# Optimization experiments

Hardware: AMD Instinct MI355X
Metric: run time of the kernel (lower is better)

Reference implementation:

```python
import jax, jax.numpy as jnp
import numpy as np

N_SAMPLES = 131072
N_FEATURES = 512
N_KERNELS = 29


def setup_inputs() -> dict:
    key = jax.random.key(0)
    k1, k2, k3 = jax.random.split(key, 3)
    Xs = jax.random.normal(k1, (N_SAMPLES, N_FEATURES), dtype=jnp.float32)
    Xt = jax.random.normal(k2, (N_SAMPLES, N_FEATURES), dtype=jnp.float32)
    # unit-sum random betas, as in the torch default constructor
    r = jax.random.uniform(k3, (N_KERNELS, 1), dtype=jnp.float32)
    betas = r / jnp.sum(r)
    return {"Xs": Xs, "Xt": Xt, "betas": betas}


def reference(Xs, Xt, betas):
    # default length-scales: gammas = 2 ** arange(-3.5, 3.75, 0.25) -> 29 kernels
    gammas = jnp.power(jnp.float32(2.0), jnp.arange(-3.5, 3.75, 0.25, dtype=jnp.float32))  # [29]

    n, f = Xs.shape
    m = (n // 2) * 2  # drop last sample if odd
    X = Xs[:m].reshape(m // 2, 2, f)  # pairs (x_{2i-1}, x_{2i})
    Y = Xt[:m].reshape(m // 2, 2, f)  # pairs (y_{2i-1}, y_{2i})

    def sq_dist(a, b):  # [P, F] -> [P]
        d = a - b
        return jnp.sum(d * d, axis=1)

    # quadruple v_i = [x, x', y, y']; distances (x,x'), (y,y'), (x,y'), (x',y)
    D = jnp.stack(
        [
            sq_dist(X[:, 0], X[:, 1]),
            sq_dist(Y[:, 0], Y[:, 1]),
            sq_dist(X[:, 0], Y[:, 1]),
            sq_dist(X[:, 1], Y[:, 0]),
        ],
        axis=1,
    )  # [P, 4]

    # K[g, p, c] = exp(-D[p, c] / (2 * gamma_g^2)) -- all 29 kernels in one broadcast
    inv_two_gamma_sq = 1.0 / (2.0 * gammas * gammas)  # [29]
    K = jnp.exp(-D[None, :, :] * inv_two_gamma_sq[:, None, None])  # [29, P, 4]

    h_u = K[..., 0] + K[..., 1] - K[..., 2] - K[..., 3]  # [29, P]
    hat_d = jnp.mean(h_u, axis=1, keepdims=True)  # [29, 1]
    return (betas.T @ hat_d).squeeze(0)  # shape (1,)
```

## Files before the change

kernel.cpp:

```cpp
#include <hip/hip_runtime.h>

#define N_SAMPLES 131072
#define N_FEAT    512
#define N_PAIRS   (N_SAMPLES / 2)
#define N_KER     29
#define PAIR_F    (2 * N_FEAT)

#define NB_MAIN   1024
#define NW_MAIN   (NB_MAIN * 4)
#define CPW_MAIN  (N_PAIRS / NW_MAIN)

struct Batch {
  float4 x0, x1, xp0, xp1, y0, y1, yp0, yp1;
};

__device__ __forceinline__ void load_batch(const float* __restrict__ Xs,
                                           const float* __restrict__ Xt,
                                           int p, int o0, Batch& b) {
  const float* x = Xs + (size_t)p * PAIR_F;
  const float* y = Xt + (size_t)p * PAIR_F;
  b.x0  = *reinterpret_cast<const float4*>(x + o0);
  b.x1  = *reinterpret_cast<const float4*>(x + o0 + 256);
  b.xp0 = *reinterpret_cast<const float4*>(x + o0 + N_FEAT);
  b.xp1 = *reinterpret_cast<const float4*>(x + o0 + N_FEAT + 256);
  b.y0  = *reinterpret_cast<const float4*>(y + o0);
  b.y1  = *reinterpret_cast<const float4*>(y + o0 + 256);
  b.yp0 = *reinterpret_cast<const float4*>(y + o0 + N_FEAT);
  b.yp1 = *reinterpret_cast<const float4*>(y + o0 + N_FEAT + 256);
}

__device__ __forceinline__ void compute_pair(const Batch& b, double c, int lane,
                                             double& acc) {
  double d0 = 0.0, d1 = 0.0, d2 = 0.0, d3 = 0.0;

#define MMD_ACC(A, AP, B, BP)                                   \
  {                                                             \
    const double ax  = (double)(A);                             \
    const double axp = (double)(AP);                            \
    const double ay  = (double)(B);                             \
    const double ayp = (double)(BP);                            \
    double t;                                                   \
    t = ax - axp; d0 = fma(t, t, d0);                           \
    t = ay - ayp; d1 = fma(t, t, d1);                           \
    t = ax - ayp; d2 = fma(t, t, d2);                           \
    t = axp - ay; d3 = fma(t, t, d3);                           \
  }
  MMD_ACC(b.x0.x, b.xp0.x, b.y0.x, b.yp0.x)
  MMD_ACC(b.x0.y, b.xp0.y, b.y0.y, b.yp0.y)
  MMD_ACC(b.x0.z, b.xp0.z, b.y0.z, b.yp0.z)
  MMD_ACC(b.x0.w, b.xp0.w, b.y0.w, b.yp0.w)
  MMD_ACC(b.x1.x, b.xp1.x, b.y1.x, b.yp1.x)
  MMD_ACC(b.x1.y, b.xp1.y, b.y1.y, b.yp1.y)
  MMD_ACC(b.x1.z, b.xp1.z, b.y1.z, b.yp1.z)
  MMD_ACC(b.x1.w, b.xp1.w, b.y1.w, b.yp1.w)
#undef MMD_ACC

#pragma unroll
  for (int s = 32; s > 0; s >>= 1) {
    d0 += __shfl_xor(d0, s);
    d1 += __shfl_xor(d1, s);
    d2 += __shfl_xor(d2, s);
    d3 += __shfl_xor(d3, s);
  }

  if (lane < N_KER) {
    acc += exp(-d0 * c) + exp(-d1 * c) - exp(-d2 * c) - exp(-d3 * c);
  }
}

__device__ __forceinline__ void block_reduce_store(double acc, int lane, int wib,
                                                   int tid, double* __restrict__ ws) {
  __shared__ double sacc[4][32];
  if (lane < 32) sacc[wib][lane] = (lane < N_KER) ? acc : 0.0;
  __syncthreads();
  if (tid < 32) {
    const double s = sacc[0][tid] + sacc[1][tid] + sacc[2][tid] + sacc[3][tid];
    ws[(size_t)blockIdx.x * 32 + tid] = s;
  }
}

__global__ __launch_bounds__(256) void mmd_partial_main(
    const float* __restrict__ Xs, const float* __restrict__ Xt,
    double* __restrict__ ws) {
  const int tid  = threadIdx.x;
  const int lane = tid & 63;
  const int wib  = tid >> 6;
  const int gw   = blockIdx.x * 4 + wib;
  const int o0   = lane * 4;

  const double c = exp2(6.0 - 0.5 * (double)lane);
  double acc = 0.0;

  int pl = gw;
  Batch A, B, C;
  load_batch(Xs, Xt, pl, o0, A); pl += NW_MAIN;
  load_batch(Xs, Xt, pl, o0, B); pl += NW_MAIN;

#pragma unroll 1
  for (int it = 0; it < (CPW_MAIN - 4) / 3; ++it) {
    load_batch(Xs, Xt, pl, o0, C); pl += NW_MAIN;
    compute_pair(A, c, lane, acc);
    load_batch(Xs, Xt, pl, o0, A); pl += NW_MAIN;
    compute_pair(B, c, lane, acc);
    load_batch(Xs, Xt, pl, o0, B); pl += NW_MAIN;
    compute_pair(C, c, lane, acc);
  }
  load_batch(Xs, Xt, pl, o0, C); pl += NW_MAIN;
  compute_pair(A, c, lane, acc);
  load_batch(Xs, Xt, pl, o0, A);
  compute_pair(B, c, lane, acc);
  compute_pair(C, c, lane, acc);
  compute_pair(A, c, lane, acc);

  block_reduce_store(acc, lane, wib, tid, ws);
}

__global__ __launch_bounds__(256) void mmd_partial_fb(
    const float* __restrict__ Xs, const float* __restrict__ Xt,
    double* __restrict__ ws, int nwaves) {
  const int tid  = threadIdx.x;
  const int lane = tid & 63;
  const int wib  = tid >> 6;
  const int gw   = blockIdx.x * 4 + wib;
  const int o0   = lane * 4;

  const double c = exp2(6.0 - 0.5 * (double)lane);
  double acc = 0.0;

  int p = gw;
  if (p < N_PAIRS) {
    Batch A, B;
    load_batch(Xs, Xt, p, o0, A);
    int pn = p + nwaves;
    bool pendingA = true;
    while (pn < N_PAIRS) {
      load_batch(Xs, Xt, pn, o0, B);
      compute_pair(A, c, lane, acc);
      pn += nwaves;
      if (pn < N_PAIRS) {
        load_batch(Xs, Xt, pn, o0, A);
        compute_pair(B, c, lane, acc);
        pn += nwaves;
      } else {
        compute_pair(B, c, lane, acc);
        pendingA = false;
        break;
      }
    }
    if (pendingA) compute_pair(A, c, lane, acc);
  }

  block_reduce_store(acc, lane, wib, tid, ws);
}

__global__ __launch_bounds__(1024) void mmd_final(
    const double* __restrict__ ws, const float* __restrict__ betas,
    float* __restrict__ out, int nb) {
  const int tid = threadIdx.x;
  double acc = 0.0;
  const int total = nb * 32;
  for (int i = tid; i < total; i += 1024) {
    const int g = i & 31;
    if (g < N_KER) acc += (double)betas[g] * ws[i];
  }
  __shared__ double s[1024];
  s[tid] = acc;
  __syncthreads();
  for (int ofs = 512; ofs > 0; ofs >>= 1) {
    if (tid < ofs) s[tid] += s[tid + ofs];
    __syncthreads();
  }
  if (tid == 0) out[0] = (float)(s[0] / (double)N_PAIRS);
}

extern "C" void kernel_launch(void* const* d_in, const int* in_sizes, int n_in,
                              void* d_out, int out_size, void* d_ws, size_t ws_size,
                              hipStream_t stream) {
  const float* Xs    = (const float*)d_in[0];
  const float* Xt    = (const float*)d_in[1];
  const float* betas = (const float*)d_in[2];
  float*  out = (float*)d_out;
  double* ws  = (double*)d_ws;

  if (ws_size >= (size_t)NB_MAIN * 32 * sizeof(double)) {
    mmd_partial_main<<<NB_MAIN, 256, 0, stream>>>(Xs, Xt, ws);
    mmd_final<<<1, 1024, 0, stream>>>(ws, betas, out, NB_MAIN);
  } else {
    size_t nb_fit = ws_size / (32 * sizeof(double));
    int nb = 1;
    while ((size_t)(nb * 2) <= nb_fit && nb * 2 <= NB_MAIN) nb *= 2;
    mmd_partial_fb<<<nb, 256, 0, stream>>>(Xs, Xt, ws, nb * 4);
    mmd_final<<<1, 1024, 0, stream>>>(ws, betas, out, nb);
  }
}
```

Before: 107.7 us.

## Partition pairs into contiguous per-XCD ranges and use two-buffer prefetch

Maps each block to an XCD through blockIdx modulo 8 and gives each XCD a contiguous slice of the pair range, so a given chiplet's waves stream neighbouring memory. This is meant to improve locality and reduce cross-XCD L2 and fabric contention for the streaming loads. The software pipeline also shrinks from triple to double buffering, which lowers register use but exposes more load latency. It relies on blocks being dispatched round-robin across XCDs.

```diff
diff --git a/kernel.cpp b/kernel.cpp
--- a/kernel.cpp
+++ b/kernel.cpp
@@ -7,8 +7,10 @@
 #define PAIR_F    (2 * N_FEAT)
 
 #define NB_MAIN   1024
-#define NW_MAIN   (NB_MAIN * 4)
-#define CPW_MAIN  (N_PAIRS / NW_MAIN)
+#define NXCD      8
+#define WPX       (NB_MAIN * 4 / NXCD)
+#define PPX       (N_PAIRS / NXCD)
+#define CPW       (PPX / WPX)
 
 struct Batch {
   float4 x0, x1, xp0, xp1, y0, y1, yp0, yp1;
@@ -79,38 +81,35 @@
   }
 }
 
-__global__ __launch_bounds__(256) void mmd_partial_main(
+__global__ __launch_bounds__(256) void mmd_partial_xcd(
     const float* __restrict__ Xs, const float* __restrict__ Xt,
     double* __restrict__ ws) {
   const int tid  = threadIdx.x;
   const int lane = tid & 63;
   const int wib  = tid >> 6;
-  const int gw   = blockIdx.x * 4 + wib;
+  const int bid  = blockIdx.x;
+  const int xcd  = bid & (NXCD - 1);
+  const int slot = bid >> 3;
+  const int wloc = slot * 4 + wib;
   const int o0   = lane * 4;
 
   const double c = exp2(6.0 - 0.5 * (double)lane);
   double acc = 0.0;
 
-  int pl = gw;
-  Batch A, B, C;
-  load_batch(Xs, Xt, pl, o0, A); pl += NW_MAIN;
-  load_batch(Xs, Xt, pl, o0, B); pl += NW_MAIN;
+  const int p0 = xcd * PPX + wloc;
+  Batch A, B;
+  load_batch(Xs, Xt, p0,       o0, A);
+  load_batch(Xs, Xt, p0 + WPX, o0, B);
 
 #pragma unroll 1
-  for (int it = 0; it < (CPW_MAIN - 4) / 3; ++it) {
-    load_batch(Xs, Xt, pl, o0, C); pl += NW_MAIN;
+  for (int k = 0; k < CPW / 2 - 1; ++k) {
     compute_pair(A, c, lane, acc);
-    load_batch(Xs, Xt, pl, o0, A); pl += NW_MAIN;
+    load_batch(Xs, Xt, p0 + (2 * k + 2) * WPX, o0, A);
     compute_pair(B, c, lane, acc);
-    load_batch(Xs, Xt, pl, o0, B); pl += NW_MAIN;
-    compute_pair(C, c, lane, acc);
+    load_batch(Xs, Xt, p0 + (2 * k + 3) * WPX, o0, B);
   }
-  load_batch(Xs, Xt, pl, o0, C); pl += NW_MAIN;
   compute_pair(A, c, lane, acc);
-  load_batch(Xs, Xt, pl, o0, A);
   compute_pair(B, c, lane, acc);
-  compute_pair(C, c, lane, acc);
-  compute_pair(A, c, lane, acc);
 
   block_reduce_store(acc, lane, wib, tid, ws);
 }
@@ -183,7 +182,7 @@
   double* ws  = (double*)d_ws;
 
   if (ws_size >= (size_t)NB_MAIN * 32 * sizeof(double)) {
-    mmd_partial_main<<<NB_MAIN, 256, 0, stream>>>(Xs, Xt, ws);
+    mmd_partial_xcd<<<NB_MAIN, 256, 0, stream>>>(Xs, Xt, ws);
     mmd_final<<<1, 1024, 0, stream>>>(ws, betas, out, NB_MAIN);
   } else {
     size_t nb_fit = ws_size / (32 * sizeof(double));
```

Result: slower. 113.5 us (+5.4%).
